# Optimization experiments

Measured on AMD Instinct MI355X. Metric: run time of the kernel, lower is better.

The kernel has to match this reference:

```python
import jax, jax.numpy as jnp
import numpy as np

N_QUBITS = 6
EPS = 1e-5
B = 65536


def _ry(t):
    # RY(t) = [[cos t/2, -sin t/2], [sin t/2, cos t/2]]; t scalar or (B,)
    c = jnp.cos(0.5 * t)
    s = jnp.sin(0.5 * t)
    row0 = jnp.stack([c, -s], -1)
    row1 = jnp.stack([s, c], -1)
    return jnp.stack([row0, row1], -2).astype(jnp.complex64)


def _rz(t):
    # RZ(t) = diag(e^{-it/2}, e^{it/2})
    e = jnp.exp(-0.5j * t)
    z = jnp.zeros_like(e)
    row0 = jnp.stack([e, z], -1)
    row1 = jnp.stack([z, jnp.conj(e)], -1)
    return jnp.stack([row0, row1], -2)


def _apply_1q(psi, U, w):
    # psi: (B, 2,...,2); U: (2,2) shared or (B,2,2) batched
    psi = jnp.moveaxis(psi, w + 1, -1)
    if U.ndim == 2:
        psi = psi @ U.T
    else:
        psi = jnp.einsum('b...i,bji->b...j', psi, U)
    return jnp.moveaxis(psi, -1, w + 1)


def _cnot(psi, c, t):
    ca, ta = c + 1, t + 1
    p0 = jnp.take(psi, 0, axis=ca)
    p1 = jnp.take(psi, 1, axis=ca)
    p1 = jnp.flip(p1, axis=ta - 1 if ta > ca else ta)  # X on target where control=1
    return jnp.stack([p0, p1], axis=ca)


def _sel(psi, theta):
    # StronglyEntanglingLayers: Rot(phi, th, om) per wire, then ring of CNOTs with range r
    n_layers = theta.shape[0]
    for l in range(n_layers):
        for w in range(N_QUBITS):
            phi, th, om = theta[l, w, 0], theta[l, w, 1], theta[l, w, 2]
            U = _rz(om) @ _ry(th) @ _rz(phi)  # Rot = RZ(om) RY(th) RZ(phi)
            psi = _apply_1q(psi, U, w)
        r = l % (N_QUBITS - 1) + 1  # PennyLane default ranges
        for w in range(N_QUBITS):
            psi = _cnot(psi, w, (w + r) % N_QUBITS)
    return psi


def setup_inputs() -> dict:
    key = jax.random.key(0)
    ks = jax.random.split(key, 11)
    d = 64
    return {
        'x': jax.random.normal(ks[0], (B, d), jnp.float32),
        'W1': jax.random.normal(ks[1], (64, d), jnp.float32) / np.sqrt(d),
        'b1': jax.random.normal(ks[2], (64,), jnp.float32) * 0.01,
        'ln_g': jnp.ones((64,), jnp.float32),
        'ln_b': jnp.zeros((64,), jnp.float32),
        'W2': jax.random.normal(ks[3], (N_QUBITS, 64), jnp.float32) / 8.0,
        'b2': jax.random.normal(ks[4], (N_QUBITS,), jnp.float32) * 0.01,
        'theta_shared': jax.random.uniform(ks[5], (2, N_QUBITS, 3), jnp.float32, 0.0, 2.0 * np.pi),
        'theta_task': jax.random.uniform(ks[6], (1, N_QUBITS, 3), jnp.float32, 0.0, 2.0 * np.pi),
        'Wc': jax.random.normal(ks[7], (5, N_QUBITS), jnp.float32) / np.sqrt(N_QUBITS),
        'bc': jnp.zeros((5,), jnp.float32),
    }


def reference(x, W1, b1, ln_g, ln_b, W2, b2, theta_shared, theta_task, Wc, bc):
    # encoder: Linear -> ReLU -> LayerNorm -> Linear -> Tanh
    h = jax.nn.relu(x @ W1.T + b1)
    mu = jnp.mean(h, -1, keepdims=True)
    var = jnp.mean((h - mu) ** 2, -1, keepdims=True)
    h = (h - mu) * jax.lax.rsqrt(var + EPS) * ln_g + ln_b
    z = jnp.tanh(h @ W2.T + b2)  # (B, 6)

    # batched 6-qubit state-vector simulator
    n = z.shape[0]
    psi = jnp.zeros((n, 2 ** N_QUBITS), jnp.complex64).at[:, 0].set(1.0)
    psi = psi.reshape((n,) + (2,) * N_QUBITS)
    ang = np.pi * z
    for w in range(N_QUBITS):
        psi = _apply_1q(psi, _ry(ang[:, w]), w)  # batched RY encoding
    psi = _sel(psi, theta_shared)
    psi = _sel(psi, theta_task)

    probs = psi.real ** 2 + psi.imag ** 2  # (n, 2,...,2)
    zvals = []
    for w in range(N_QUBITS):
        pw = jnp.moveaxis(probs, w + 1, 1).reshape(n, 2, -1).sum(-1)
        zvals.append(pw[:, 0] - pw[:, 1])  # <Z_w>
    q = jnp.stack(zvals, -1)  # (n, 6)
    return q @ Wc.T + bc
```

## Files before the change

kernel.cpp:

```cpp
#include <hip/hip_runtime.h>
#include <math.h>

#define NQ 6
#define DIM 64
#define W1S 65
#define PI_F 3.14159265358979323846f

template <int CTRL, int ROWM, bool BC>
__device__ __forceinline__ float dpp_add_src(float v) {
  int r = __builtin_amdgcn_update_dpp(0, __float_as_int(v), CTRL, ROWM, 0xF, BC);
  return __int_as_float(r);
}

__device__ __forceinline__ float red_sum(float v) {
  v += dpp_add_src<0x111, 0xF, true>(v);
  v += dpp_add_src<0x112, 0xF, true>(v);
  v += dpp_add_src<0x114, 0xF, true>(v);
  v += dpp_add_src<0x118, 0xF, true>(v);
  v += dpp_add_src<0x142, 0xA, false>(v);
  v += dpp_add_src<0x143, 0xC, false>(v);
  return v;
}
__device__ __forceinline__ float bcast63(float v) {
  return __int_as_float(__builtin_amdgcn_readlane(__float_as_int(v), 63));
}
__device__ __forceinline__ float rdlane(float v, int l) {
  return __int_as_float(__builtin_amdgcn_readlane(__float_as_int(v), l));
}

template <int W>
__device__ __forceinline__ float sh_partner(float v) {
  if constexpr (W == 5) {
    int i = __float_as_int(v);
    return __int_as_float(__builtin_amdgcn_update_dpp(i, i, 0xB1, 0xF, 0xF, false));
  } else if constexpr (W == 4) {
    int i = __float_as_int(v);
    return __int_as_float(__builtin_amdgcn_update_dpp(i, i, 0x4E, 0xF, 0xF, false));
  } else if constexpr (W == 3) {
    return __int_as_float(__builtin_amdgcn_ds_swizzle(__float_as_int(v), 0x101F));
  } else if constexpr (W == 2) {
    return __int_as_float(__builtin_amdgcn_ds_swizzle(__float_as_int(v), 0x201F));
  } else if constexpr (W == 1) {
    return __int_as_float(__builtin_amdgcn_ds_swizzle(__float_as_int(v), 0x401F));
  } else {
    return __shfl_xor(v, 32, 64);
  }
}

template <int W>
__device__ __forceinline__ void gate_w(float& re, float& im, float4 c, int lane) {
  float pr = sh_partner<W>(re);
  float pi = sh_partner<W>(im);
  const bool hi = (lane & (32 >> W)) != 0;
  float sa = hi ? -c.y : c.y;
  float sb = hi ? -c.z : c.z;
  float nr = c.x * re;
  nr = fmaf(-sa, im, nr);
  nr = fmaf(sb, pr, nr);
  nr = fmaf(-c.w, pi, nr);
  float ni = c.x * im;
  ni = fmaf(sa, re, ni);
  ni = fmaf(sb, pi, ni);
  ni = fmaf(c.w, pr, ni);
  re = nr; im = ni;
}

__device__ __forceinline__ void sel_layer(float& re, float& im,
                                          const float4* cf, int pa, int lane) {
  gate_w<0>(re, im, cf[0], lane);
  gate_w<1>(re, im, cf[1], lane);
  gate_w<2>(re, im, cf[2], lane);
  gate_w<3>(re, im, cf[3], lane);
  gate_w<4>(re, im, cf[4], lane);
  gate_w<5>(re, im, cf[5], lane);
  re = __int_as_float(__builtin_amdgcn_ds_bpermute(pa, __float_as_int(re)));
  im = __int_as_float(__builtin_amdgcn_ds_bpermute(pa, __float_as_int(im)));
}

__device__ __forceinline__ int cnot_src(int j, int r) {
  int i = j;
  #pragma unroll
  for (int w = 5; w >= 0; --w) {
    const int cm = 32 >> w;
    const int tm = 32 >> ((w + r) % NQ);
    if (i & cm) i ^= tm;
  }
  return i;
}

__global__ __launch_bounds__(256) void qmaml_wave(
    const float* __restrict__ x,
    const float* __restrict__ W1,
    const float* __restrict__ b1,
    const float* __restrict__ ln_g,
    const float* __restrict__ ln_b,
    const float* __restrict__ W2,
    const float* __restrict__ b2,
    const float* __restrict__ th_sh,
    const float* __restrict__ th_tk,
    const float* __restrict__ Wc,
    const float* __restrict__ bc,
    float* __restrict__ out,
    int B)
{
  __shared__ float w1t[64 * W1S];
  __shared__ float4 coef[18];

  const int tid = threadIdx.x;

  #pragma unroll
  for (int it = 0; it < 16; ++it) {
    int idx = tid + it * 256;
    int j = idx >> 6, k = idx & 63;
    w1t[k * W1S + j] = W1[idx];
  }
  if (tid < 18) {
    const int layer = tid / 6, w = tid % 6;
    const float* th = (layer < 2) ? (th_sh + (layer * 6 + w) * 3)
                                  : (th_tk + w * 3);
    const float phi = th[0], the = th[1], om = th[2];
    float S, C;   sincosf(0.5f * the,        &S,  &C);
    float sS, cS; sincosf(0.5f * (om + phi), &sS, &cS);
    float sD, cD; sincosf(0.5f * (om - phi), &sD, &cD);
    coef[tid] = make_float4(C * cS, -C * sS, -S * cD, S * sD);
  }
  __syncthreads();

  const int lane = tid & 63;
  const int gw = blockIdx.x * 4 + (tid >> 6);
  const int nw = gridDim.x * 4;

  const float b1v = b1[lane];
  const float lgv = ln_g[lane];
  const float lbv = ln_b[lane];
  float w2v[NQ];
  #pragma unroll
  for (int m = 0; m < NQ; ++m) w2v[m] = W2[m * DIM + lane];
  const float b2v = (lane < NQ) ? b2[lane] : 0.0f;
  const float bcv = (lane < 5) ? bc[lane] : 0.0f;
  float g[5];
  #pragma unroll
  for (int j = 0; j < 5; ++j) {
    float a = 0.0f;
    #pragma unroll
    for (int w = 0; w < NQ; ++w) {
      float wc = Wc[j * NQ + w];
      a += (lane & (32 >> w)) ? -wc : wc;
    }
    g[j] = a;
  }
  const int pa1 = cnot_src(lane, 1) << 2;
  const int pa2 = cnot_src(lane, 2) << 2;

  for (int t = gw; t < B; t += nw) {
    const float* __restrict__ xr =
        x + (size_t)__builtin_amdgcn_readfirstlane(t) * DIM;

    float acc = b1v;
    #pragma unroll
    for (int k = 0; k < DIM; ++k)
      acc = fmaf(w1t[k * W1S + lane], xr[k], acc);
    float h = fmaxf(acc, 0.0f);

    const float mu = bcast63(red_sum(h)) * (1.0f / DIM);
    const float d = h - mu;
    const float var = bcast63(red_sum(d * d)) * (1.0f / DIM);
    const float rs = __builtin_amdgcn_rsqf(var + 1e-5f);
    h = fmaf(d * rs, lgv, lbv);

    float y = 0.0f;
    #pragma unroll
    for (int m = 0; m < NQ; ++m) {
      float r = bcast63(red_sum(w2v[m] * h));
      y = (lane == m) ? r : y;
    }
    y += b2v;

    const float e = __expf(2.0f * y);
    const float tz = fmaf(-2.0f, __builtin_amdgcn_rcpf(e + 1.0f), 1.0f);
    const float ha = (0.5f * PI_F) * tz;
    const float sv = __sinf(ha);
    const float cv = __cosf(ha);
    float s[NQ], c[NQ];
    #pragma unroll
    for (int w = 0; w < NQ; ++w) { s[w] = rdlane(sv, w); c[w] = rdlane(cv, w); }

    float re = (lane & 32) ? s[0] : c[0];
    re *= (lane & 16) ? s[1] : c[1];
    re *= (lane &  8) ? s[2] : c[2];
    re *= (lane &  4) ? s[3] : c[3];
    re *= (lane &  2) ? s[4] : c[4];
    re *= (lane &  1) ? s[5] : c[5];
    float im = 0.0f;

    sel_layer(re, im, coef + 0,  pa1, lane);
    sel_layer(re, im, coef + 6,  pa2, lane);
    sel_layer(re, im, coef + 12, pa1, lane);

    const float p = fmaf(re, re, im * im);
    float o0 = bcast63(red_sum(p * g[0]));
    float o1 = bcast63(red_sum(p * g[1]));
    float o2 = bcast63(red_sum(p * g[2]));
    float o3 = bcast63(red_sum(p * g[3]));
    float o4 = bcast63(red_sum(p * g[4]));
    float vout = (lane == 0) ? o0 :
                 (lane == 1) ? o1 :
                 (lane == 2) ? o2 :
                 (lane == 3) ? o3 : o4;
    if (lane < 5) out[(size_t)t * 5 + lane] = vout + bcv;
  }
}

extern "C" void kernel_launch(void* const* d_in, const int* in_sizes, int n_in,
                              void* d_out, int out_size, void* d_ws, size_t ws_size,
                              hipStream_t stream) {
  const float* x     = (const float*)d_in[0];
  const float* W1    = (const float*)d_in[1];
  const float* b1    = (const float*)d_in[2];
  const float* ln_g  = (const float*)d_in[3];
  const float* ln_b  = (const float*)d_in[4];
  const float* W2    = (const float*)d_in[5];
  const float* b2    = (const float*)d_in[6];
  const float* th_sh = (const float*)d_in[7];
  const float* th_tk = (const float*)d_in[8];
  const float* Wc    = (const float*)d_in[9];
  const float* bc    = (const float*)d_in[10];
  float* out = (float*)d_out;

  const int B = in_sizes[0] / DIM;
  int blocks = (B + 3) / 4;
  if (blocks > 2048) blocks = 2048;
  qmaml_wave<<<blocks, 256, 0, stream>>>(x, W1, b1, ln_g, ln_b, W2, b2,
                                         th_sh, th_tk, Wc, bc, out, B);
}
```

Measured before the change: 64.61 us.

## Process four batch rows per wave to amortize W1 LDS reads and shuffles

Each wave now handles four samples per iteration. Every W1 value read from LDS is reused across four rows, and the tanh, sin and cos work is packed into one lane-parallel pass over 24 lanes. LayerNorm variance switches to the one-pass E[h^2]-mu^2 form so the two reductions can run independently. The cross-half-wave partner exchange uses permlane32_swap when the builtin is available. These raise instruction-level parallelism at the cost of more registers and lower occupancy, and the one-pass variance can lose precision.

```diff
diff --git a/kernel.cpp b/kernel.cpp
--- a/kernel.cpp
+++ b/kernel.cpp
@@ -4,7 +4,10 @@
 #define NQ 6
 #define DIM 64
 #define W1S 65
+#define NB 4
 #define PI_F 3.14159265358979323846f
+
+typedef int i32x2 __attribute__((ext_vector_type(2)));
 
 template <int CTRL, int ROWM, bool BC>
 __device__ __forceinline__ float dpp_add_src(float v) {
@@ -26,6 +29,16 @@
 }
 __device__ __forceinline__ float rdlane(float v, int l) {
   return __int_as_float(__builtin_amdgcn_readlane(__float_as_int(v), l));
+}
+
+__device__ __forceinline__ float partner32(float v, bool lo32) {
+#if __has_builtin(__builtin_amdgcn_permlane32_swap)
+  i32x2 r = __builtin_amdgcn_permlane32_swap(__float_as_int(v),
+                                             __float_as_int(v), false, false);
+  return __int_as_float(lo32 ? r[1] : r[0]);
+#else
+  return __shfl_xor(v, 32, 64);
+#endif
 }
 
 template <int W>
@@ -40,41 +53,53 @@
     return __int_as_float(__builtin_amdgcn_ds_swizzle(__float_as_int(v), 0x101F));
   } else if constexpr (W == 2) {
     return __int_as_float(__builtin_amdgcn_ds_swizzle(__float_as_int(v), 0x201F));
-  } else if constexpr (W == 1) {
+  } else {
     return __int_as_float(__builtin_amdgcn_ds_swizzle(__float_as_int(v), 0x401F));
-  } else {
-    return __shfl_xor(v, 32, 64);
   }
 }
 
 template <int W>
-__device__ __forceinline__ void gate_w(float& re, float& im, float4 c, int lane) {
-  float pr = sh_partner<W>(re);
-  float pi = sh_partner<W>(im);
-  const bool hi = (lane & (32 >> W)) != 0;
-  float sa = hi ? -c.y : c.y;
-  float sb = hi ? -c.z : c.z;
-  float nr = c.x * re;
-  nr = fmaf(-sa, im, nr);
-  nr = fmaf(sb, pr, nr);
-  nr = fmaf(-c.w, pi, nr);
-  float ni = c.x * im;
-  ni = fmaf(sa, re, ni);
-  ni = fmaf(sb, pi, ni);
-  ni = fmaf(c.w, pr, ni);
-  re = nr; im = ni;
-}
-
-__device__ __forceinline__ void sel_layer(float& re, float& im,
-                                          const float4* cf, int pa, int lane) {
-  gate_w<0>(re, im, cf[0], lane);
-  gate_w<1>(re, im, cf[1], lane);
-  gate_w<2>(re, im, cf[2], lane);
-  gate_w<3>(re, im, cf[3], lane);
-  gate_w<4>(re, im, cf[4], lane);
-  gate_w<5>(re, im, cf[5], lane);
-  re = __int_as_float(__builtin_amdgcn_ds_bpermute(pa, __float_as_int(re)));
-  im = __int_as_float(__builtin_amdgcn_ds_bpermute(pa, __float_as_int(im)));
+__device__ __forceinline__ void gate4(float (&re)[NB], float (&im)[NB],
+                                      float4 c, int lane, bool lo32) {
+  const bool hi = (W == 0) ? !lo32 : ((lane & (32 >> W)) != 0);
+  const float sa = hi ? -c.y : c.y;
+  const float sb = hi ? -c.z : c.z;
+  #pragma unroll
+  for (int r = 0; r < NB; ++r) {
+    float pr, pi;
+    if constexpr (W == 0) {
+      pr = partner32(re[r], lo32);
+      pi = partner32(im[r], lo32);
+    } else {
+      pr = sh_partner<W>(re[r]);
+      pi = sh_partner<W>(im[r]);
+    }
+    float nr = c.x * re[r];
+    nr = fmaf(-sa, im[r], nr);
+    nr = fmaf(sb, pr, nr);
+    nr = fmaf(-c.w, pi, nr);
+    float ni = c.x * im[r];
+    ni = fmaf(sa, re[r], ni);
+    ni = fmaf(sb, pi, ni);
+    ni = fmaf(c.w, pr, ni);
+    re[r] = nr; im[r] = ni;
+  }
+}
+
+__device__ __forceinline__ void sel_layer4(float (&re)[NB], float (&im)[NB],
+                                           const float4* cf, int pa,
+                                           int lane, bool lo32) {
+  gate4<0>(re, im, cf[0], lane, lo32);
+  gate4<1>(re, im, cf[1], lane, lo32);
+  gate4<2>(re, im, cf[2], lane, lo32);
+  gate4<3>(re, im, cf[3], lane, lo32);
+  gate4<4>(re, im, cf[4], lane, lo32);
+  gate4<5>(re, im, cf[5], lane, lo32);
+  #pragma unroll
+  for (int r = 0; r < NB; ++r) {
+    re[r] = __int_as_float(__builtin_amdgcn_ds_bpermute(pa, __float_as_int(re[r])));
+    im[r] = __int_as_float(__builtin_amdgcn_ds_bpermute(pa, __float_as_int(im[r])));
+  }
 }
 
 __device__ __forceinline__ int cnot_src(int j, int r) {
@@ -88,7 +113,7 @@
   return i;
 }
 
-__global__ __launch_bounds__(256) void qmaml_wave(
+__global__ __launch_bounds__(256, 4) void qmaml_wave4(
     const float* __restrict__ x,
     const float* __restrict__ W1,
     const float* __restrict__ b1,
@@ -111,8 +136,7 @@
   #pragma unroll
   for (int it = 0; it < 16; ++it) {
     int idx = tid + it * 256;
-    int j = idx >> 6, k = idx & 63;
-    w1t[k * W1S + j] = W1[idx];
+    w1t[(idx & 63) * W1S + (idx >> 6)] = W1[idx];
   }
   if (tid < 18) {
     const int layer = tid / 6, w = tid % 6;
@@ -127,7 +151,8 @@
   __syncthreads();
 
   const int lane = tid & 63;
-  const int gw = blockIdx.x * 4 + (tid >> 6);
+  const bool lo32 = lane < 32;
+  const int wid = __builtin_amdgcn_readfirstlane(blockIdx.x * 4 + (tid >> 6));
   const int nw = gridDim.x * 4;
 
   const float b1v = b1[lane];
@@ -136,7 +161,7 @@
   float w2v[NQ];
   #pragma unroll
   for (int m = 0; m < NQ; ++m) w2v[m] = W2[m * DIM + lane];
-  const float b2v = (lane < NQ) ? b2[lane] : 0.0f;
+  const float b2p = (lane < NB * NQ) ? b2[lane % NQ] : 0.0f;
   const float bcv = (lane < 5) ? bc[lane] : 0.0f;
   float g[5];
   #pragma unroll
@@ -152,62 +177,79 @@
   const int pa1 = cnot_src(lane, 1) << 2;
   const int pa2 = cnot_src(lane, 2) << 2;
 
-  for (int t = gw; t < B; t += nw) {
-    const float* __restrict__ xr =
-        x + (size_t)__builtin_amdgcn_readfirstlane(t) * DIM;
-
-    float acc = b1v;
-    #pragma unroll
-    for (int k = 0; k < DIM; ++k)
-      acc = fmaf(w1t[k * W1S + lane], xr[k], acc);
-    float h = fmaxf(acc, 0.0f);
-
-    const float mu = bcast63(red_sum(h)) * (1.0f / DIM);
-    const float d = h - mu;
-    const float var = bcast63(red_sum(d * d)) * (1.0f / DIM);
-    const float rs = __builtin_amdgcn_rsqf(var + 1e-5f);
-    h = fmaf(d * rs, lgv, lbv);
+  for (int t0 = wid * NB; t0 < B; t0 += nw * NB) {
+    float acc[NB];
+    const float* xp[NB];
+    #pragma unroll
+    for (int r = 0; r < NB; ++r) {
+      int tr = t0 + r; if (tr > B - 1) tr = B - 1;
+      xp[r] = x + (size_t)tr * DIM;
+      acc[r] = b1v;
+    }
+    #pragma unroll
+    for (int k = 0; k < DIM; ++k) {
+      const float wv = w1t[k * W1S + lane];
+      #pragma unroll
+      for (int r = 0; r < NB; ++r) acc[r] = fmaf(wv, xp[r][k], acc[r]);
+    }
+
+    float h[NB];
+    #pragma unroll
+    for (int r = 0; r < NB; ++r) {
+      const float hv = fmaxf(acc[r], 0.0f);
+      const float s1 = bcast63(red_sum(hv)) * (1.0f / DIM);
+      const float s2 = bcast63(red_sum(hv * hv)) * (1.0f / DIM);
+      const float var = s2 - s1 * s1;
+      const float rs = __builtin_amdgcn_rsqf(var + 1e-5f);
+      h[r] = fmaf((hv - s1) * rs, lgv, lbv);
+    }
 
     float y = 0.0f;
     #pragma unroll
     for (int m = 0; m < NQ; ++m) {
-      float r = bcast63(red_sum(w2v[m] * h));
-      y = (lane == m) ? r : y;
-    }
-    y += b2v;
+      #pragma unroll
+      for (int r = 0; r < NB; ++r) {
+        const float s = bcast63(red_sum(w2v[m] * h[r]));
+        y = (lane == r * NQ + m) ? s : y;
+      }
+    }
+    y += b2p;
 
     const float e = __expf(2.0f * y);
     const float tz = fmaf(-2.0f, __builtin_amdgcn_rcpf(e + 1.0f), 1.0f);
     const float ha = (0.5f * PI_F) * tz;
     const float sv = __sinf(ha);
     const float cv = __cosf(ha);
-    float s[NQ], c[NQ];
-    #pragma unroll
-    for (int w = 0; w < NQ; ++w) { s[w] = rdlane(sv, w); c[w] = rdlane(cv, w); }
-
-    float re = (lane & 32) ? s[0] : c[0];
-    re *= (lane & 16) ? s[1] : c[1];
-    re *= (lane &  8) ? s[2] : c[2];
-    re *= (lane &  4) ? s[3] : c[3];
-    re *= (lane &  2) ? s[4] : c[4];
-    re *= (lane &  1) ? s[5] : c[5];
-    float im = 0.0f;
-
-    sel_layer(re, im, coef + 0,  pa1, lane);
-    sel_layer(re, im, coef + 6,  pa2, lane);
-    sel_layer(re, im, coef + 12, pa1, lane);
-
-    const float p = fmaf(re, re, im * im);
-    float o0 = bcast63(red_sum(p * g[0]));
-    float o1 = bcast63(red_sum(p * g[1]));
-    float o2 = bcast63(red_sum(p * g[2]));
-    float o3 = bcast63(red_sum(p * g[3]));
-    float o4 = bcast63(red_sum(p * g[4]));
-    float vout = (lane == 0) ? o0 :
-                 (lane == 1) ? o1 :
-                 (lane == 2) ? o2 :
-                 (lane == 3) ? o3 : o4;
-    if (lane < 5) out[(size_t)t * 5 + lane] = vout + bcv;
+
+    float re[NB], im[NB];
+    #pragma unroll
+    for (int r = 0; r < NB; ++r) {
+      float a = (lane & 32) ? rdlane(sv, r * NQ + 0) : rdlane(cv, r * NQ + 0);
+      a *= (lane & 16) ? rdlane(sv, r * NQ + 1) : rdlane(cv, r * NQ + 1);
+      a *= (lane &  8) ? rdlane(sv, r * NQ + 2) : rdlane(cv, r * NQ + 2);
+      a *= (lane &  4) ? rdlane(sv, r * NQ + 3) : rdlane(cv, r * NQ + 3);
+      a *= (lane &  2) ? rdlane(sv, r * NQ + 4) : rdlane(cv, r * NQ + 4);
+      a *= (lane &  1) ? rdlane(sv, r * NQ + 5) : rdlane(cv, r * NQ + 5);
+      re[r] = a;
+      im[r] = 0.0f;
+    }
+
+    sel_layer4(re, im, coef + 0,  pa1, lane, lo32);
+    sel_layer4(re, im, coef + 6,  pa2, lane, lo32);
+    sel_layer4(re, im, coef + 12, pa1, lane, lo32);
+
+    #pragma unroll
+    for (int r = 0; r < NB; ++r) {
+      const float p = fmaf(re[r], re[r], im[r] * im[r]);
+      float vout = 0.0f;
+      #pragma unroll
+      for (int j = 0; j < 5; ++j) {
+        const float o = bcast63(red_sum(p * g[j]));
+        vout = (lane == j) ? o : vout;
+      }
+      const int tr = t0 + r;
+      if (lane < 5 && tr < B) out[(size_t)tr * 5 + lane] = vout + bcv;
+    }
   }
 }
 
@@ -228,8 +270,8 @@
   float* out = (float*)d_out;
 
   const int B = in_sizes[0] / DIM;
-  int blocks = (B + 3) / 4;
+  int blocks = (B + 16 - 1) / 16;
   if (blocks > 2048) blocks = 2048;
-  qmaml_wave<<<blocks, 256, 0, stream>>>(x, W1, b1, ln_g, ln_b, W2, b2,
-                                         th_sh, th_tk, Wc, bc, out, B);
-}
+  qmaml_wave4<<<blocks, 256, 0, stream>>>(x, W1, b1, ln_g, ln_b, W2, b2,
+                                          th_sh, th_tk, Wc, bc, out, B);
+}
```

Result: slower. 96.90 us (+50.0%).
